# Optimization experiments

Hardware: AMD Instinct MI355X
Metric: run time of the kernel (lower is better)

The kernel has to match this reference:

```python
import jax, jax.numpy as jnp
import numpy as np

N = 50000      # nodes
E = 800000     # edges (avg degree 16)
F_IN = 256     # input feature dim
H, D = 4, 32   # heads, per-head dim
HD = H * D
K = 25000      # SAGPool keeps ceil(0.5*N) nodes
C = 2          # classes
SLOPE = 0.4
NEG = -1e9

def _gat(x, src, dst, valid, n, W, b, al, ar):
    # DGL GATConv: fc -> per-head attn logits -> edge softmax over dst -> weighted sum
    h = (x @ W).reshape(-1, H, D)                      # [n,H,D]
    el = jnp.einsum('nhd,hd->nh', h, al)
    er = jnp.einsum('nhd,hd->nh', h, ar)
    e = jax.nn.leaky_relu(el[src] + er[dst], SLOPE)    # [E,H]
    e = jnp.where(valid[:, None], e, NEG)
    m = jnp.maximum(jax.ops.segment_max(e, dst, num_segments=n), NEG)
    ex = jnp.exp(e - m[dst]) * valid[:, None].astype(x.dtype)
    s = jax.ops.segment_sum(ex, dst, num_segments=n)
    alpha = ex / jnp.maximum(s[dst], 1e-16)            # [E,H] edge softmax
    out = jax.ops.segment_sum(alpha[:, :, None] * h[src], dst, num_segments=n)
    return out + b.reshape(1, H, D), alpha

def _sagpool(x, src, dst, valid, n, k, Wc, bc):
    # score = GraphConv(in,1) with symmetric norm; keep top-k nodes, scale by tanh(score)
    vf = valid.astype(x.dtype)
    deg_o = jnp.maximum(jax.ops.segment_sum(vf, src, num_segments=n), 1.0)
    deg_i = jnp.maximum(jax.ops.segment_sum(vf, dst, num_segments=n), 1.0)
    h = (x @ Wc) * (deg_o ** -0.5)[:, None]
    agg = jax.ops.segment_sum(h[src] * vf[:, None], dst, num_segments=n)
    score = (agg * (deg_i ** -0.5)[:, None] + bc)[:, 0]   # [n]
    vals, perm = jax.lax.top_k(score, k)
    xk = x[perm] * jnp.tanh(vals)[:, None]                # [k,F]
    new_id = jnp.full((n,), -1, jnp.int32).at[perm].set(jnp.arange(k, dtype=jnp.int32))
    ns, nd = new_id[src], new_id[dst]
    nv = valid & (ns >= 0) & (nd >= 0)                    # edges fully inside subgraph
    return xk, jnp.where(nv, ns, 0), jnp.where(nv, nd, 0), nv

def setup_inputs():
    key = jax.random.key(0)
    k = jax.random.split(key, 18)
    rn = lambda i, shape, scale: jax.random.normal(k[i], shape, jnp.float32) * scale
    return {
        "feature": rn(0, (N, F_IN), 1.0),
        "strength": jax.random.uniform(k[1], (E,), dtype=jnp.float32),
        "W0": rn(2, (F_IN, HD), F_IN ** -0.5), "b0": jnp.zeros((HD,), jnp.float32),
        "al0": rn(3, (H, D), 0.1), "ar0": rn(4, (H, D), 0.1),
        "Wc0": rn(5, (HD, 1), HD ** -0.5), "bc0": jnp.zeros((1,), jnp.float32),
        "W1": rn(6, (HD, HD), HD ** -0.5), "b1": jnp.zeros((HD,), jnp.float32),
        "al1": rn(7, (H, D), 0.1), "ar1": rn(8, (H, D), 0.1),
        "gate_W": rn(9, (D, 1), D ** -0.5), "gate_b": jnp.zeros((1,), jnp.float32),
        "cls_W": rn(10, (D, C), D ** -0.5), "cls_b": jnp.zeros((C,), jnp.float32),
        "src": jax.random.randint(k[11], (E,), 0, N, dtype=jnp.int32),
        "dst": jax.random.randint(k[12], (E,), 0, N, dtype=jnp.int32),
    }

def reference(feature, strength, W0, b0, al0, ar0, Wc0, bc0, W1, b1, al1, ar1,
              gate_W, gate_b, cls_W, cls_b, src, dst):
    valid0 = jnp.ones((E,), bool)
    h0, _ = _gat(feature, src, dst, valid0, N, W0, b0, al0, ar0)
    x = h0.reshape(N, HD)                                  # flatten(1)
    x1, s1, d1, v1 = _sagpool(x, src, dst, valid0, N, K, Wc0, bc0)
    h1, atten = _gat(x1, s1, d1, v1, K, W1, b1, al1, ar1)  # get_attention=True
    strength1 = strength * v1.astype(strength.dtype)       # edata carried into subgraph (masked)
    res = h1.mean(axis=1)                                  # [K,D] mean over heads
    gate = jax.nn.softmax(res @ gate_W + gate_b, axis=0)   # [K,1] GlobalAttentionPooling
    readout = jnp.sum(gate * res, axis=0, keepdims=True)   # [1,D]
    lbl_pred = readout @ cls_W + cls_b                     # [1,C]
    return (readout, lbl_pred, atten, strength1)
```

## Files before the change

### kernel.cpp

```cpp
#include <hip/hip_runtime.h>
#include <stdint.h>

#define NN 50000
#define EE 800000
#define FIN 256
#define HD 128
#define DD 32
#define KK 25000
#define SLOPEF 0.4f
#define NEGF (-1e9f)
#define ATT_OFF 34
#define STR_OFF (34 + EE * 4)
#define CW 128

#define BCH 32
#define EPC (EE / BCH)

__device__ __forceinline__ unsigned fkey(float x) {
    unsigned u = __float_as_uint(x);
    return (u & 0x80000000u) ? ~u : (u | 0x80000000u);
}
__device__ __forceinline__ float unfkey(unsigned k) {
    unsigned u = (k & 0x80000000u) ? (k ^ 0x80000000u) : ~k;
    return __uint_as_float(u);
}
__device__ __forceinline__ float lrelu(float v) { return v > 0.f ? v : SLOPEF * v; }

struct P {
    const float *feature, *strength, *W0, *b0, *al0, *ar0, *Wc0, *bc0;
    const float *W1, *b1, *al1, *ar1, *gW, *gb, *cW, *cb;
    const int *src, *dst;
    double *Zacc, *racc;
    int *cnt;
    unsigned *gmaxk;
    unsigned *rs;
    unsigned *binsHi, *binsLo;
    unsigned *keys;
    unsigned char *degc_i, *degc_o;
    unsigned *cb0;
    int *dsum;
    int *csr_src, *rank, *off0, *sel, *slot, *list, *bsum, *boff;
    float *z0, *el0, *er0, *q4, *m0f, *s0f, *b0wc, *hc, *xk, *z1;
    float *el1, *er1, *m1f, *s1f, *res, *g, *tscale;
    float *out;
};

#define BM 128
#define BN 64
#define BK 16
__device__ void gemm_body(
    const float* __restrict__ A, const float* __restrict__ B, float* __restrict__ C,
    int M, int Kd,
    const float* __restrict__ al, const float* __restrict__ ar,
    float* __restrict__ el, float* __restrict__ er,
    const float* __restrict__ Wc, float* __restrict__ q4,
    int bx, int by) {
    __shared__ float As[BK][BM + 4];
    __shared__ float Bs[BK][BN];
    int bm = by * BM, bn = bx * BN;
    int tid = threadIdx.x;
    int tr = tid >> 4, tc = tid & 15;
    int lrow = tid >> 1;
    int arow = (bm + lrow < M) ? (bm + lrow) : -1;
    float acc[8][4] = {};
    for (int k0 = 0; k0 < Kd; k0 += BK) {
        {
            int col = (tid & 1) << 3;
            float4 v0 = {0.f,0.f,0.f,0.f}, v1 = {0.f,0.f,0.f,0.f};
            if (arow >= 0) {
                const float* ap = A + (size_t)arow * Kd + k0 + col;
                v0 = *(const float4*)ap; v1 = *(const float4*)(ap + 4);
            }
            As[col + 0][lrow] = v0.x; As[col + 1][lrow] = v0.y;
            As[col + 2][lrow] = v0.z; As[col + 3][lrow] = v0.w;
            As[col + 4][lrow] = v1.x; As[col + 5][lrow] = v1.y;
            As[col + 6][lrow] = v1.z; As[col + 7][lrow] = v1.w;
        }
        {
            int kr = tid >> 4, col = (tid & 15) << 2;
            float4 v = *(const float4*)(B + (size_t)(k0 + kr) * HD + bn + col);
            *(float4*)&Bs[kr][col] = v;
        }
        __syncthreads();
#pragma unroll
        for (int kk = 0; kk < BK; kk++) {
            float a[8], b[4];
#pragma unroll
            for (int i = 0; i < 8; i++) a[i] = As[kk][tr * 8 + i];
#pragma unroll
            for (int j = 0; j < 4; j++) b[j] = Bs[kk][tc * 4 + j];
#pragma unroll
            for (int i = 0; i < 8; i++)
#pragma unroll
                for (int j = 0; j < 4; j++) acc[i][j] = fmaf(a[i], b[j], acc[i][j]);
        }
        __syncthreads();
    }
#pragma unroll
    for (int i = 0; i < 8; i++) {
        int gr = bm + tr * 8 + i;
        if (gr < M) {
            float4 v = {acc[i][0], acc[i][1], acc[i][2], acc[i][3]};
            *(float4*)(C + (size_t)gr * HD + bn + tc * 4) = v;
        }
    }
    int head = bx * 2 + (tc >> 3);
    int dbase = (tc & 7) * 4;
    const float* alh = al + head * 32 + dbase;
    const float* arh = ar + head * 32 + dbase;
    float a0 = alh[0], a1 = alh[1], a2 = alh[2], a3 = alh[3];
    float r0 = arh[0], r1 = arh[1], r2 = arh[2], r3 = arh[3];
    float w0 = 0.f, w1 = 0.f, w2 = 0.f, w3 = 0.f;
    if (Wc) {
        const float* wch = Wc + head * 32 + dbase;
        w0 = wch[0]; w1 = wch[1]; w2 = wch[2]; w3 = wch[3];
    }
#pragma unroll
    for (int i = 0; i < 8; i++) {
        int gr = bm + tr * 8 + i;
        float pe = acc[i][0]*a0 + acc[i][1]*a1 + acc[i][2]*a2 + acc[i][3]*a3;
        float pr = acc[i][0]*r0 + acc[i][1]*r1 + acc[i][2]*r2 + acc[i][3]*r3;
        float pq = acc[i][0]*w0 + acc[i][1]*w1 + acc[i][2]*w2 + acc[i][3]*w3;
#pragma unroll
        for (int o = 1; o < 8; o <<= 1) {
            pe += __shfl_xor(pe, o); pr += __shfl_xor(pr, o); pq += __shfl_xor(pq, o);
        }
        if ((tc & 7) == 0 && gr < M) {
            el[gr * 4 + head] = pe; er[gr * 4 + head] = pr;
            if (Wc) q4[gr * 4 + head] = pq;
        }
    }
}

__global__ __launch_bounds__(256) void k_count0(P p) {
    __shared__ unsigned hist[NN / 4];
    int blk = blockIdx.x;
    int isD = blk < BCH;
    int c = isD ? blk : blk - BCH;
    for (int w = threadIdx.x; w < NN / 4; w += 256) hist[w] = 0u;
    __syncthreads();
    int j0 = c * EPC, j1 = j0 + EPC;
    if (isD) {
        for (int e = j0 + (int)threadIdx.x; e < j1; e += 256) {
            int d = p.dst[e];
            unsigned sh = (unsigned)(d & 3) * 8u;
            unsigned old = atomicAdd(&hist[d >> 2], 1u << sh);
            p.rank[e] = (int)((old >> sh) & 0xffu);
        }
    } else {
        for (int e = j0 + (int)threadIdx.x; e < j1; e += 256) {
            int s = p.src[e];
            atomicAdd(&hist[s >> 2], 1u << ((unsigned)(s & 3) * 8u));
        }
    }
    __syncthreads();
    unsigned* o32 = (unsigned*)((isD ? p.degc_i : p.degc_o) + (size_t)c * NN);
    for (int w = threadIdx.x; w < NN / 4; w += 256) o32[w] = hist[w];
}

__global__ __launch_bounds__(256) void k_bsum(const unsigned char* __restrict__ deg,
                                              int* __restrict__ bsum, int n, int nn) {
    int i = blockIdx.x * 256 + threadIdx.x;
    int v = 0;
    if (i < n) {
#pragma unroll
        for (int c = 0; c < BCH; c++) v += deg[(size_t)c * nn + i];
    }
    int lane = threadIdx.x & 63, w = threadIdx.x >> 6;
    __shared__ int ws[4];
#pragma unroll
    for (int o = 1; o < 64; o <<= 1) v += __shfl_xor(v, o);
    if (lane == 0) ws[w] = v;
    __syncthreads();
    if (threadIdx.x == 0) bsum[blockIdx.x] = ws[0] + ws[1] + ws[2] + ws[3];
}
__global__ __launch_bounds__(256) void k_bscan(const int* __restrict__ bsum, int nb,
                                               int* __restrict__ boff,
                                               int* __restrict__ off, int n) {
    __shared__ int ws[4];
    __shared__ int wo[5];
    int t = threadIdx.x;
    int v = (t < nb) ? bsum[t] : 0;
    int lane = t & 63, w = t >> 6;
    int incl = v;
    for (int o = 1; o < 64; o <<= 1) { int u = __shfl_up(incl, o); if (lane >= o) incl += u; }
    if (lane == 63) ws[w] = incl;
    __syncthreads();
    if (t == 0) { int a = 0; for (int i = 0; i < 4; i++) { wo[i] = a; a += ws[i]; } wo[4] = a; }
    __syncthreads();
    if (t < nb) boff[t] = wo[w] + incl - v;
    if (t == 0) off[n] = wo[4];
}
__global__ __launch_bounds__(256) void k_fscan0(P p) {
    __shared__ int ws[4];
    __shared__ int wo[4];
    int i = blockIdx.x * 256 + threadIdx.x;
    int v = 0;
    if (i < NN) {
#pragma unroll
        for (int c = 0; c < BCH; c++) v += p.degc_i[(size_t)c * NN + i];
    }
    int lane = threadIdx.x & 63, w = threadIdx.x >> 6;
    int incl = v;
    for (int o = 1; o < 64; o <<= 1) { int u = __shfl_up(incl, o); if (lane >= o) incl += u; }
    if (lane == 63) ws[w] = incl;
    __syncthreads();
    if (threadIdx.x == 0) { int a = 0; for (int k = 0; k < 4; k++) { wo[k] = a; a += ws[k]; } }
    __syncthreads();
    if (i < NN) {
        int base = p.boff[blockIdx.x] + wo[w] + incl - v;
        p.off0[i] = base;
        unsigned run = (unsigned)base;
        int s = 0;
#pragma unroll
        for (int c = 0; c < BCH; c++) {
            p.cb0[(size_t)c * NN + i] = run;
            run += p.degc_i[(size_t)c * NN + i];
            s += p.degc_o[(size_t)c * NN + i];
        }
        p.dsum[i] = s;
    }
}

#define G0B 782
#define GB_E 3125
__global__ __launch_bounds__(256) void k_g0sc(P p) {
    int blk = blockIdx.x;
    if (blk < G0B) {
        gemm_body(p.feature, p.W0, p.z0, NN, FIN, p.al0, p.ar0, p.el0, p.er0,
                  p.Wc0, p.q4, blk & 1, blk >> 1);
    } else if (blk < G0B + GB_E) {
        int e = (blk - G0B) * 256 + threadIdx.x;
        if (e < EE) {
            int c = e / EPC;
            int d = p.dst[e];
            unsigned pos = p.cb0[(size_t)c * NN + d] + (unsigned)p.rank[e];
            p.csr_src[pos] = p.src[e];
        }
    } else {
        int l = threadIdx.x;
        if (l < 64) {
            float t = p.b0[l] * p.Wc0[l] + p.b0[l + 64] * p.Wc0[l + 64];
#pragma unroll
            for (int o = 1; o < 64; o <<= 1) t += __shfl_xor(t, o);
            if (l == 0) p.b0wc[0] = t;
        }
    }
}

__global__ __launch_bounds__(256) void k_fgatlite(
    const int* __restrict__ off, const int* __restrict__ csrs,
    const float* __restrict__ el, const float* __restrict__ er,
    const float* __restrict__ q4, const int* __restrict__ dsum,
    const float* __restrict__ b0wc,
    float* __restrict__ hc, float* __restrict__ m0f, float* __restrict__ s0f) {
    int wv = threadIdx.x >> 6, lane = threadIdx.x & 63;
    int v = blockIdx.x * 4 + wv;
    int b = off[v], e = off[v + 1], deg = e - b;
    int h = lane >> 4, sub = lane & 15;
    float erh = er[(size_t)v * 4 + h];
    float m = NEGF;
    for (int li = sub; li < deg; li += 16) {
        int s = csrs[b + li];
        m = fmaxf(m, lrelu(el[(size_t)s * 4 + h] + erh));
    }
#pragma unroll
    for (int o = 1; o < 16; o <<= 1) m = fmaxf(m, __shfl_xor(m, o));
    float ssum = 0.f, hq = 0.f;
    for (int li = sub; li < deg; li += 16) {
        int s = csrs[b + li];
        float ex = expf(lrelu(el[(size_t)s * 4 + h] + erh) - m);
        ssum += ex;
        hq = fmaf(ex, q4[(size_t)s * 4 + h], hq);
    }
#pragma unroll
    for (int o = 1; o < 16; o <<= 1) { ssum += __shfl_xor(ssum, o); hq += __shfl_xor(hq, o); }
    if (sub == 0) { m0f[v * 4 + h] = m; s0f[v * 4 + h] = ssum; }
    float t = hq / fmaxf(ssum, 1e-16f);
    t += __shfl_xor(t, 16);
    t += __shfl_xor(t, 32);
    if (lane == 0)
        hc[v] = (t + b0wc[0]) / sqrtf(fmaxf((float)dsum[v], 1.f));
}

__global__ __launch_bounds__(256) void k_score(P p) {
    int v = blockIdx.x * blockDim.x + threadIdx.x;
    if (v >= NN) return;
    int b = p.off0[v], en = p.off0[v + 1];
    float acc = 0.f;
    for (int i = b; i < en; i++) acc += p.hc[p.csr_src[i]];
    float dg = fmaxf((float)(en - b), 1.f);
    float sc = acc / sqrtf(dg) + p.bc0[0];
    p.keys[v] = fkey(sc);
    p.sel[v] = 0;
}

#define HB 49
__global__ __launch_bounds__(1024) void k_h0(P p) {
    __shared__ unsigned hist[16384];
    int i = blockIdx.x * 1024 + (int)threadIdx.x;
    unsigned key = (i < NN) ? p.keys[i] : 0xFFFFFFFFu;
    unsigned b16 = key >> 16;
#pragma unroll
    for (int half = 0; half < 2; half++) {
        for (int w = threadIdx.x; w < 16384; w += 1024) hist[w] = 0u;
        __syncthreads();
        if (i < NN && (int)(b16 >> 15) == half) {
            unsigned bb = b16 & 0x7FFFu;
            atomicAdd(&hist[bb >> 1], 1u << (16u * (bb & 1u)));
        }
        __syncthreads();
        for (int w = threadIdx.x; w < 16384; w += 1024) {
            unsigned hv = hist[w];
            unsigned lo = hv & 0xFFFFu, hi = hv >> 16;
            if (lo) atomicAdd(&p.binsHi[half * 32768 + 2 * w], lo);
            if (hi) atomicAdd(&p.binsHi[half * 32768 + 2 * w + 1], hi);
        }
        __syncthreads();
    }
}

__global__ __launch_bounds__(1024) void k_h1(P p) {
    __shared__ unsigned hist[16384];
    int i = blockIdx.x * 1024 + (int)threadIdx.x;
    unsigned hib = p.rs[2];
    unsigned key = (i < NN) ? p.keys[i] : 0u;
    int cand = (i < NN) && ((key >> 16) == hib);
    unsigned b16 = key & 0xFFFFu;
#pragma unroll
    for (int half = 0; half < 2; half++) {
        for (int w = threadIdx.x; w < 16384; w += 1024) hist[w] = 0u;
        __syncthreads();
        if (cand && (int)(b16 >> 15) == half) {
            unsigned bb = b16 & 0x7FFFu;
            atomicAdd(&hist[bb >> 1], 1u << (16u * (bb & 1u)));
        }
        __syncthreads();
        for (int w = threadIdx.x; w < 16384; w += 1024) {
            unsigned hv = hist[w];
            unsigned lo = hv & 0xFFFFu, hi = hv >> 16;
            if (lo) atomicAdd(&p.binsLo[half * 32768 + 2 * w], lo);
            if (hi) atomicAdd(&p.binsLo[half * 32768 + 2 * w + 1], hi);
        }
        __syncthreads();
    }
}

__global__ __launch_bounds__(1024) void k_rsel2(P p, int level) {
    const unsigned* bins = level ? p.binsLo : p.binsHi;
    int K = level ? (int)p.rs[3] : KK;
    __shared__ unsigned wsm[16];
    __shared__ unsigned wpre[17];
    int t = threadIdx.x;
    unsigned base = (unsigned)t * 64;
    const uint4* b4 = (const uint4*)(bins + base);
    unsigned S = 0;
#pragma unroll
    for (int i = 0; i < 16; i++) {
        uint4 u = b4[i];
        S += u.x + u.y + u.z + u.w;
    }
    int lane = t & 63, w = t >> 6;
    unsigned val = S;
    for (int o = 1; o < 64; o <<= 1) { unsigned u = __shfl_up(val, o); if (lane >= o) val += u; }
    if (lane == 63) wsm[w] = val;
    __syncthreads();
    if (t == 0) { unsigned a = 0; for (int i = 0; i < 16; i++) { wpre[i] = a; a += wsm[i]; } wpre[16] = a; }
    __syncthreads();
    unsigned incl = wpre[w] + val;
    unsigned running = wpre[16] - incl;
    for (int i = 63; i >= 0; i--) {
        unsigned c = bins[base + i];
        unsigned above = running;
        running += c;
        if ((int)above < K && (int)running >= K) {
            if (level == 0) { p.rs[2] = base + (unsigned)i; p.rs[3] = (unsigned)(K - (int)above); }
            else { p.rs[0] = (p.rs[2] << 16) | (base + (unsigned)i); p.rs[1] = (unsigned)(K - (int)above); }
        }
    }
}

__global__ __launch_bounds__(1024) void k_ties(P p) {
    __shared__ int base;
    __shared__ int wsums[16];
    unsigned pivot = p.rs[0];
    int need = (int)p.rs[1];
    if (threadIdx.x == 0) base = 0;
    __syncthreads();
    for (int st = 0; st < NN; st += 1024) {
        int v = st + (int)threadIdx.x;
        int flag = (v < NN && p.keys[v] == pivot) ? 1 : 0;
        unsigned long long m = __ballot(flag);
        int lane = threadIdx.x & 63, w = threadIdx.x >> 6;
        int pre = __popcll(m & ((1ull << lane) - 1ull));
        if (lane == 0) wsums[w] = __popcll(m);
        __syncthreads();
        int woff = 0;
        for (int i = 0; i < w; i++) woff += wsums[i];
        int rank = base + woff + pre;
        if (flag && rank < need) p.sel[v] = 1;
        __syncthreads();
        if (threadIdx.x == 0) {
            int s = 0;
            for (int i = 0; i < 16; i++) s += wsums[i];
            base += s;
        }
        __syncthreads();
    }
}

__global__ void k_list(P p) {
    int v = blockIdx.x * blockDim.x + threadIdx.x;
    if (v >= NN) return;
    unsigned k = p.keys[v];
    int selv = (k > p.rs[0]) || p.sel[v];
    if (selv) {
        int i = atomicAdd(p.cnt, 1);
        p.list[i] = v;
        p.slot[v] = i;
        p.tscale[i] = tanhf(unfkey(k));
    } else {
        p.slot[v] = -1;
    }
}

__global__ __launch_bounds__(256) void k_fgatx(
    const int* __restrict__ list, const float* __restrict__ tscale,
    const int* __restrict__ off, const int* __restrict__ csrs,
    const float* __restrict__ el, const float* __restrict__ er,
    const float* __restrict__ m0f, const float* __restrict__ s0f,
    const float* __restrict__ z, const float* __restrict__ b0,
    float* __restrict__ xk) {
    __shared__ int ssrc[4][CW];
    __shared__ float sexp[4][CW][4];
    int wv = threadIdx.x >> 6, lane = threadIdx.x & 63;
    int i = blockIdx.x * 4 + wv;
    int v = list[i];
    int b = off[v], e = off[v + 1], deg = e - b;
    int h = lane >> 4, sub = lane & 15;
    float erh = er[(size_t)v * 4 + h];
    float mh = m0f[v * 4 + h];
    for (int li = sub; li < deg; li += 16) {
        int s = csrs[b + li];
        if (h == 0 && li < CW) ssrc[wv][li] = s;
        if (li < CW) sexp[wv][li][h] = expf(lrelu(el[(size_t)s * 4 + h] + erh) - mh);
    }
    __syncthreads();
    int h0 = lane >> 5, h1 = h0 + 2;
    float s0 = s0f[v * 4 + h0], s1 = s0f[v * 4 + h1];
    float m0 = m0f[v * 4 + h0], m1 = m0f[v * 4 + h1];
    float er0v = er[(size_t)v * 4 + h0], er1v = er[(size_t)v * 4 + h1];
    int c0 = lane, c1 = lane + 64;
    float acc0 = 0.f, acc1 = 0.f;
    for (int li = 0; li < deg; li++) {
        int s; float w0, w1;
        if (li < CW) {
            s = ssrc[wv][li];
            w0 = sexp[wv][li][h0]; w1 = sexp[wv][li][h1];
        } else {
            s = csrs[b + li];
            w0 = expf(lrelu(el[(size_t)s * 4 + h0] + er0v) - m0);
            w1 = expf(lrelu(el[(size_t)s * 4 + h1] + er1v) - m1);
        }
        int su = __builtin_amdgcn_readfirstlane(s);
        const float* zr = z + (size_t)su * HD;
        acc0 = fmaf(w0, zr[c0], acc0);
        acc1 = fmaf(w1, zr[c1], acc1);
    }
    float ts = tscale[i];
    float* xr = xk + (size_t)i * HD;
    xr[c0] = (acc0 / fmaxf(s0, 1e-16f) + b0[c0]) * ts;
    xr[c1] = (acc1 / fmaxf(s1, 1e-16f) + b0[c1]) * ts;
}

#define G1B 392
__global__ __launch_bounds__(256) void k_gemm1(P p) {
    gemm_body(p.xk, p.W1, p.z1, KK, HD, p.al1, p.ar1, p.el1, p.er1,
              nullptr, nullptr, blockIdx.x & 1, blockIdx.x >> 1);
}

__global__ __launch_bounds__(256) void k_fgat2(P p) {
    __shared__ int ssrc[4][CW];
    __shared__ float sexp[4][CW][4];
    int wv = threadIdx.x >> 6, lane = threadIdx.x & 63;
    int i = blockIdx.x * 4 + wv;
    int v = p.list[i];
    int b = p.off0[v], e = p.off0[v + 1], deg = e - b;
    int h = lane >> 4, sub = lane & 15;
    float4 er4 = *(const float4*)(p.er1 + (size_t)i * 4);
    float erh = ((const float*)&er4)[h];
    float m = NEGF;
    for (int li = sub; li < deg; li += 16) {
        int so = p.csr_src[b + li];
        int ss = p.slot[so];
        if (h == 0 && li < CW) ssrc[wv][li] = ss;
        if (ss >= 0) m = fmaxf(m, lrelu(p.el1[(size_t)ss * 4 + h] + erh));
    }
#pragma unroll
    for (int o = 1; o < 16; o <<= 1) m = fmaxf(m, __shfl_xor(m, o));
    float ssum = 0.f;
    for (int li = sub; li < deg; li += 16) {
        int so = p.csr_src[b + li];
        int ss = p.slot[so];
        float x = (ss >= 0) ? expf(lrelu(p.el1[(size_t)ss * 4 + h] + erh) - m) : 0.f;
        if (li < CW) sexp[wv][li][h] = x;
        ssum += x;
    }
#pragma unroll
    for (int o = 1; o < 16; o <<= 1) ssum += __shfl_xor(ssum, o);
    if (sub == 0) { p.m1f[i * 4 + h] = m; p.s1f[i * 4 + h] = ssum; }
    __syncthreads();
    int h0 = lane >> 5, h1 = h0 + 2;
    float m0 = __shfl(m, h0 << 4), m1 = __shfl(m, h1 << 4);
    float s0 = __shfl(ssum, h0 << 4), s1 = __shfl(ssum, h1 << 4);
    int c0 = lane, c1 = lane + 64;
    float acc0 = 0.f, acc1 = 0.f;
    for (int li = 0; li < deg; li++) {
        int s; float w0, w1;
        if (li < CW) {
            s = ssrc[wv][li];
            if (s < 0) continue;
            w0 = sexp[wv][li][h0]; w1 = sexp[wv][li][h1];
        } else {
            int so = p.csr_src[b + li];
            s = p.slot[so];
            if (s < 0) continue;
            w0 = expf(lrelu(p.el1[(size_t)s * 4 + h0] + ((const float*)&er4)[h0]) - m0);
            w1 = expf(lrelu(p.el1[(size_t)s * 4 + h1] + ((const float*)&er4)[h1]) - m1);
        }
        int su = __builtin_amdgcn_readfirstlane(s);
        const float* zr = p.z1 + (size_t)su * HD;
        acc0 = fmaf(w0, zr[c0], acc0);
        acc1 = fmaf(w1, zr[c1], acc1);
    }
    float xc0 = acc0 / fmaxf(s0, 1e-16f) + p.b1[c0];
    float xc1 = acc1 / fmaxf(s1, 1e-16f) + p.b1[c1];
    float t = xc0 + xc1;
    t += __shfl_xor(t, 32);
    float pg = 0.f;
    if (lane < 32) {
        float r = 0.25f * t;
        p.res[(size_t)i * 32 + lane] = r;
        pg = r * p.gW[lane];
    }
#pragma unroll
    for (int o = 1; o < 32; o <<= 1) pg += __shfl_xor(pg, o);
    if (lane == 0) p.g[i] = pg + p.gb[0];
}

__global__ void k_ealpha1(P p) {
    int e = blockIdx.x * blockDim.x + threadIdx.x;
    if (e >= EE) return;
    int ds = p.slot[p.src[e]], dd = p.slot[p.dst[e]];
    float a[4] = {0.f, 0.f, 0.f, 0.f};
    float st = 0.f;
    if (ds >= 0 && dd >= 0) {
        float4 es = *(const float4*)(p.el1 + ds * 4);
        float4 ed = *(const float4*)(p.er1 + dd * 4);
        float l[4] = {lrelu(es.x + ed.x), lrelu(es.y + ed.y), lrelu(es.z + ed.z), lrelu(es.w + ed.w)};
#pragma unroll
        for (int h = 0; h < 4; h++) {
            float m = p.m1f[dd * 4 + h];
            float ex = expf(l[h] - m);
            a[h] = ex / fmaxf(p.s1f[dd * 4 + h], 1e-16f);
        }
        st = p.strength[e];
    }
    float* o = p.out + ATT_OFF + (size_t)e * 4;
    *(float2*)(o) = make_float2(a[0], a[1]);
    *(float2*)(o + 2) = make_float2(a[2], a[3]);
    p.out[STR_OFF + e] = st;
}

__global__ void k_gmax(P p) {
    __shared__ float red[256];
    int t = threadIdx.x;
    float m = -3.4e38f;
    for (int i = blockIdx.x * 256 + t; i < KK; i += gridDim.x * 256) m = fmaxf(m, p.g[i]);
    red[t] = m;
    __syncthreads();
    for (int o = 128; o > 0; o >>= 1) { if (t < o) red[t] = fmaxf(red[t], red[t + o]); __syncthreads(); }
    if (t == 0) atomicMax(p.gmaxk, fkey(red[0]));
}
#define WSUM_BLOCKS 104
__global__ __launch_bounds__(256) void k_wsum(P p) {
    __shared__ double vred[256];
    __shared__ double zred[8];
    int t = threadIdx.x, il = t >> 5, d = t & 31;
    float gm = unfkey(*p.gmaxk);
    double accv = 0.0, accw = 0.0;
    for (int i = blockIdx.x * 8 + il; i < KK; i += WSUM_BLOCKS * 8) {
        float w = expf(p.g[i] - gm);
        accv += (double)(w * p.res[(size_t)i * 32 + d]);
        if (d == 0) accw += (double)w;
    }
    vred[t] = accv;
    if (d == 0) zred[il] = accw;
    __syncthreads();
    if (il == 0) {
        double s = 0;
#pragma unroll
        for (int k2 = 0; k2 < 8; k2++) s += vred[k2 * 32 + d];
        atomicAdd(&p.racc[d], s);
    }
    if (t == 32) {
        double z2 = 0;
#pragma unroll
        for (int k2 = 0; k2 < 8; k2++) z2 += zred[k2];
        atomicAdd(p.Zacc, z2);
    }
}
__global__ void k_final(P p) {
    __shared__ float rb[32];
    int t = threadIdx.x;
    double Z = *p.Zacc;
    if (t < 32) {
        float r = (float)(p.racc[t] / Z);
        p.out[t] = r;
        rb[t] = r;
    }
    __syncthreads();
    if (t < 2) {
        float s = 0.f;
        for (int d = 0; d < 32; d++) s += rb[d] * p.cW[d * 2 + t];
        p.out[32 + t] = s + p.cb[t];
    }
}

extern "C" void kernel_launch(void* const* d_in, const int* in_sizes, int n_in,
                              void* d_out, int out_size, void* d_ws, size_t ws_size,
                              hipStream_t stream) {
    (void)in_sizes; (void)n_in; (void)out_size; (void)ws_size;
    P p;
    p.feature  = (const float*)d_in[0];
    p.strength = (const float*)d_in[1];
    p.W0  = (const float*)d_in[2];  p.b0  = (const float*)d_in[3];
    p.al0 = (const float*)d_in[4];  p.ar0 = (const float*)d_in[5];
    p.Wc0 = (const float*)d_in[6];  p.bc0 = (const float*)d_in[7];
    p.W1  = (const float*)d_in[8];  p.b1  = (const float*)d_in[9];
    p.al1 = (const float*)d_in[10]; p.ar1 = (const float*)d_in[11];
    p.gW  = (const float*)d_in[12]; p.gb  = (const float*)d_in[13];
    p.cW  = (const float*)d_in[14]; p.cb  = (const float*)d_in[15];
    p.src = (const int*)d_in[16];   p.dst = (const int*)d_in[17];
    p.out = (float*)d_out;

    char* ws = (char*)d_ws;
    size_t off = 0;
    auto alloc = [&](size_t bytes) -> void* {
        void* r = ws + off;
        off = (off + bytes + 255) & ~(size_t)255;
        return r;
    };
    p.Zacc  = (double*)alloc(8);
    p.racc  = (double*)alloc(32 * 8);
    p.cnt   = (int*)alloc(4);
    p.gmaxk = (unsigned*)alloc(4);
    p.rs    = (unsigned*)alloc(16);
    p.binsHi = (unsigned*)alloc(65536 * 4);
    p.binsLo = (unsigned*)alloc(65536 * 4);
    size_t zbytes = off;
    p.degc_i = (unsigned char*)alloc((size_t)BCH * NN);
    p.degc_o = (unsigned char*)alloc((size_t)BCH * NN);
    p.cb0 = (unsigned*)alloc((size_t)BCH * NN * 4);
    p.dsum = (int*)alloc((size_t)NN * 4);
    p.z0 = (float*)alloc((size_t)NN * HD * 4);
    p.xk = (float*)alloc((size_t)KK * HD * 4);
    p.z1 = (float*)alloc((size_t)KK * HD * 4);
    p.csr_src = (int*)alloc((size_t)EE * 4);
    p.rank    = (int*)alloc((size_t)EE * 4);
    p.el0 = (float*)alloc((size_t)NN * 4 * 4);
    p.er0 = (float*)alloc((size_t)NN * 4 * 4);
    p.q4  = (float*)alloc((size_t)NN * 4 * 4);
    p.m0f = (float*)alloc((size_t)NN * 4 * 4);
    p.s0f = (float*)alloc((size_t)NN * 4 * 4);
    p.b0wc = (float*)alloc(4);
    p.off0 = (int*)alloc((size_t)(NN + 1) * 4);
    p.bsum = (int*)alloc(256 * 4);
    p.boff = (int*)alloc(256 * 4);
    p.hc    = (float*)alloc((size_t)NN * 4);
    p.keys  = (unsigned*)alloc((size_t)NN * 4);
    p.sel   = (int*)alloc((size_t)NN * 4);
    p.slot  = (int*)alloc((size_t)NN * 4);
    p.list  = (int*)alloc((size_t)KK * 4);
    p.tscale = (float*)alloc((size_t)KK * 4);
    p.el1 = (float*)alloc((size_t)KK * 4 * 4);
    p.er1 = (float*)alloc((size_t)KK * 4 * 4);
    p.m1f = (float*)alloc((size_t)KK * 4 * 4);
    p.s1f = (float*)alloc((size_t)KK * 4 * 4);
    p.res = (float*)alloc((size_t)KK * DD * 4);
    p.g   = (float*)alloc((size_t)KK * 4);

    const int GB_N = (NN + 255) / 256;

    hipMemsetAsync(d_ws, 0, zbytes, stream);

    k_count0<<<2 * BCH, 256, 0, stream>>>(p);
    k_bsum<<<GB_N, 256, 0, stream>>>(p.degc_i, p.bsum, NN, NN);
    k_bscan<<<1, 256, 0, stream>>>(p.bsum, GB_N, p.boff, p.off0, NN);
    k_fscan0<<<GB_N, 256, 0, stream>>>(p);
    k_g0sc<<<G0B + GB_E + 1, 256, 0, stream>>>(p);
    k_fgatlite<<<NN / 4, 256, 0, stream>>>(p.off0, p.csr_src, p.el0, p.er0, p.q4,
                                           p.dsum, p.b0wc, p.hc, p.m0f, p.s0f);

    k_score<<<GB_N, 256, 0, stream>>>(p);
    k_h0<<<HB, 1024, 0, stream>>>(p);
    k_rsel2<<<1, 1024, 0, stream>>>(p, 0);
    k_h1<<<HB, 1024, 0, stream>>>(p);
    k_rsel2<<<1, 1024, 0, stream>>>(p, 1);
    k_ties<<<1, 1024, 0, stream>>>(p);
    k_list<<<GB_N, 256, 0, stream>>>(p);

    k_fgatx<<<KK / 4, 256, 0, stream>>>(p.list, p.tscale, p.off0, p.csr_src,
                                        p.el0, p.er0, p.m0f, p.s0f, p.z0, p.b0, p.xk);
    k_gemm1<<<G1B, 256, 0, stream>>>(p);
    k_fgat2<<<KK / 4, 256, 0, stream>>>(p);
    k_ealpha1<<<GB_E, 256, 0, stream>>>(p);

    k_gmax<<<98, 256, 0, stream>>>(p);
    k_wsum<<<WSUM_BLOCKS, 256, 0, stream>>>(p);
    k_final<<<1, 64, 0, stream>>>(p);
}
```

Baseline: 579.7 us.

## Parallelize degree counting, tie selection, and fuse edge-alpha with gate max

After: 532.6 us. 8.1% less time.

```diff
diff --git a/kernel.cpp b/kernel.cpp
--- a/kernel.cpp
+++ b/kernel.cpp
@@ -15,6 +15,7 @@
 
 #define BCH 32
 #define EPC (EE / BCH)
+#define NRQ 12500
 
 __device__ __forceinline__ unsigned fkey(float x) {
     unsigned u = __float_as_uint(x);
@@ -39,7 +40,7 @@
     unsigned char *degc_i, *degc_o;
     unsigned *cb0;
     int *dsum;
-    int *csr_src, *rank, *off0, *sel, *slot, *list, *bsum, *boff;
+    int *csr_src, *rank, *off0, *slot, *list, *bsum, *boff;
     float *z0, *el0, *er0, *q4, *m0f, *s0f, *b0wc, *hc, *xk, *z1;
     float *el1, *er1, *m1f, *s1f, *res, *g, *tscale;
     float *out;
@@ -133,29 +134,33 @@
 }
 
 __global__ __launch_bounds__(256) void k_count0(P p) {
-    __shared__ unsigned hist[NN / 4];
+    __shared__ unsigned hist[NRQ / 4];
     int blk = blockIdx.x;
-    int isD = blk < BCH;
-    int c = isD ? blk : blk - BCH;
-    for (int w = threadIdx.x; w < NN / 4; w += 256) hist[w] = 0u;
+    int isD = blk < 128;
+    int c = blk & 31, rq = (blk >> 5) & 3;
+    int nbase = rq * NRQ;
+    for (int w = threadIdx.x; w < NRQ / 4; w += 256) hist[w] = 0u;
     __syncthreads();
     int j0 = c * EPC, j1 = j0 + EPC;
     if (isD) {
         for (int e = j0 + (int)threadIdx.x; e < j1; e += 256) {
-            int d = p.dst[e];
-            unsigned sh = (unsigned)(d & 3) * 8u;
-            unsigned old = atomicAdd(&hist[d >> 2], 1u << sh);
-            p.rank[e] = (int)((old >> sh) & 0xffu);
+            int d = p.dst[e] - nbase;
+            if ((unsigned)d < (unsigned)NRQ) {
+                unsigned sh = (unsigned)(d & 3) * 8u;
+                unsigned old = atomicAdd(&hist[d >> 2], 1u << sh);
+                p.rank[e] = (int)((old >> sh) & 0xffu);
+            }
         }
     } else {
         for (int e = j0 + (int)threadIdx.x; e < j1; e += 256) {
-            int s = p.src[e];
-            atomicAdd(&hist[s >> 2], 1u << ((unsigned)(s & 3) * 8u));
-        }
-    }
-    __syncthreads();
-    unsigned* o32 = (unsigned*)((isD ? p.degc_i : p.degc_o) + (size_t)c * NN);
-    for (int w = threadIdx.x; w < NN / 4; w += 256) o32[w] = hist[w];
+            int s = p.src[e] - nbase;
+            if ((unsigned)s < (unsigned)NRQ)
+                atomicAdd(&hist[s >> 2], 1u << ((unsigned)(s & 3) * 8u));
+        }
+    }
+    __syncthreads();
+    unsigned* o32 = (unsigned*)((isD ? p.degc_i : p.degc_o) + (size_t)c * NN + nbase);
+    for (int w = threadIdx.x; w < NRQ / 4; w += 256) o32[w] = hist[w];
 }
 
 __global__ __launch_bounds__(256) void k_bsum(const unsigned char* __restrict__ deg,
@@ -222,21 +227,22 @@
     }
 }
 
+#define GB_E 3125
+__global__ __launch_bounds__(256) void k_scat0(P p) {
+    int e = blockIdx.x * 256 + threadIdx.x;
+    if (e >= EE) return;
+    int c = e / EPC;
+    int d = p.dst[e];
+    unsigned pos = p.cb0[(size_t)c * NN + d] + (unsigned)p.rank[e];
+    p.csr_src[pos] = p.src[e];
+}
+
 #define G0B 782
-#define GB_E 3125
-__global__ __launch_bounds__(256) void k_g0sc(P p) {
+__global__ __launch_bounds__(256) void k_gemm0(P p) {
     int blk = blockIdx.x;
     if (blk < G0B) {
         gemm_body(p.feature, p.W0, p.z0, NN, FIN, p.al0, p.ar0, p.el0, p.er0,
                   p.Wc0, p.q4, blk & 1, blk >> 1);
-    } else if (blk < G0B + GB_E) {
-        int e = (blk - G0B) * 256 + threadIdx.x;
-        if (e < EE) {
-            int c = e / EPC;
-            int d = p.dst[e];
-            unsigned pos = p.cb0[(size_t)c * NN + d] + (unsigned)p.rank[e];
-            p.csr_src[pos] = p.src[e];
-        }
     } else {
         int l = threadIdx.x;
         if (l < 64) {
@@ -292,7 +298,6 @@
     float dg = fmaxf((float)(en - b), 1.f);
     float sc = acc / sqrtf(dg) + p.bc0[0];
     p.keys[v] = fkey(sc);
-    p.sel[v] = 0;
 }
 
 #define HB 49
@@ -380,47 +385,48 @@
     }
 }
 
-__global__ __launch_bounds__(1024) void k_ties(P p) {
-    __shared__ int base;
-    __shared__ int wsums[16];
+__global__ __launch_bounds__(256) void k_tcnt(P p) {
+    __shared__ int ws[4];
+    int v = blockIdx.x * 256 + (int)threadIdx.x;
+    int flag = (v < NN && p.keys[v] == p.rs[0]) ? 1 : 0;
+    unsigned long long m = __ballot(flag);
+    int lane = threadIdx.x & 63, w = threadIdx.x >> 6;
+    if (lane == 0) ws[w] = __popcll(m);
+    __syncthreads();
+    if (threadIdx.x == 0) p.bsum[blockIdx.x] = ws[0] + ws[1] + ws[2] + ws[3];
+}
+
+__global__ __launch_bounds__(256) void k_list(P p) {
+    __shared__ int pre0;
+    __shared__ int ws[4];
+    int blk = blockIdx.x, tid = threadIdx.x;
     unsigned pivot = p.rs[0];
     int need = (int)p.rs[1];
-    if (threadIdx.x == 0) base = 0;
-    __syncthreads();
-    for (int st = 0; st < NN; st += 1024) {
-        int v = st + (int)threadIdx.x;
-        int flag = (v < NN && p.keys[v] == pivot) ? 1 : 0;
-        unsigned long long m = __ballot(flag);
-        int lane = threadIdx.x & 63, w = threadIdx.x >> 6;
-        int pre = __popcll(m & ((1ull << lane) - 1ull));
-        if (lane == 0) wsums[w] = __popcll(m);
-        __syncthreads();
-        int woff = 0;
-        for (int i = 0; i < w; i++) woff += wsums[i];
-        int rank = base + woff + pre;
-        if (flag && rank < need) p.sel[v] = 1;
-        __syncthreads();
-        if (threadIdx.x == 0) {
-            int s = 0;
-            for (int i = 0; i < 16; i++) s += wsums[i];
-            base += s;
-        }
-        __syncthreads();
-    }
-}
-
-__global__ void k_list(P p) {
-    int v = blockIdx.x * blockDim.x + threadIdx.x;
-    if (v >= NN) return;
-    unsigned k = p.keys[v];
-    int selv = (k > p.rs[0]) || p.sel[v];
-    if (selv) {
-        int i = atomicAdd(p.cnt, 1);
-        p.list[i] = v;
-        p.slot[v] = i;
-        p.tscale[i] = tanhf(unfkey(k));
-    } else {
-        p.slot[v] = -1;
+    int v = blk * 256 + tid;
+    unsigned k = (v < NN) ? p.keys[v] : 0u;
+    int flag = (v < NN && k == pivot) ? 1 : 0;
+    unsigned long long mask = __ballot(flag);
+    int lane = tid & 63, w = tid >> 6;
+    if (lane == 0) ws[w] = __popcll(mask);
+    if (tid == 0) {
+        int s = 0;
+        for (int b2 = 0; b2 < blk; b2++) s += p.bsum[b2];
+        pre0 = s;
+    }
+    __syncthreads();
+    int woff = 0;
+    for (int i = 0; i < w; i++) woff += ws[i];
+    int rank = pre0 + woff + __popcll(mask & ((1ull << lane) - 1ull));
+    if (v < NN) {
+        int selv = (k > pivot) || (flag && rank < need);
+        if (selv) {
+            int idx = atomicAdd(p.cnt, 1);
+            p.list[idx] = v;
+            p.slot[v] = idx;
+            p.tscale[idx] = tanhf(unfkey(k));
+        } else {
+            p.slot[v] = -1;
+        }
     }
 }
 
@@ -548,40 +554,42 @@
     if (lane == 0) p.g[i] = pg + p.gb[0];
 }
 
-__global__ void k_ealpha1(P p) {
-    int e = blockIdx.x * blockDim.x + threadIdx.x;
-    if (e >= EE) return;
-    int ds = p.slot[p.src[e]], dd = p.slot[p.dst[e]];
-    float a[4] = {0.f, 0.f, 0.f, 0.f};
-    float st = 0.f;
-    if (ds >= 0 && dd >= 0) {
-        float4 es = *(const float4*)(p.el1 + ds * 4);
-        float4 ed = *(const float4*)(p.er1 + dd * 4);
-        float l[4] = {lrelu(es.x + ed.x), lrelu(es.y + ed.y), lrelu(es.z + ed.z), lrelu(es.w + ed.w)};
-#pragma unroll
-        for (int h = 0; h < 4; h++) {
-            float m = p.m1f[dd * 4 + h];
-            float ex = expf(l[h] - m);
-            a[h] = ex / fmaxf(p.s1f[dd * 4 + h], 1e-16f);
-        }
-        st = p.strength[e];
-    }
-    float* o = p.out + ATT_OFF + (size_t)e * 4;
-    *(float2*)(o) = make_float2(a[0], a[1]);
-    *(float2*)(o + 2) = make_float2(a[2], a[3]);
-    p.out[STR_OFF + e] = st;
-}
-
-__global__ void k_gmax(P p) {
-    __shared__ float red[256];
-    int t = threadIdx.x;
-    float m = -3.4e38f;
-    for (int i = blockIdx.x * 256 + t; i < KK; i += gridDim.x * 256) m = fmaxf(m, p.g[i]);
-    red[t] = m;
-    __syncthreads();
-    for (int o = 128; o > 0; o >>= 1) { if (t < o) red[t] = fmaxf(red[t], red[t + o]); __syncthreads(); }
-    if (t == 0) atomicMax(p.gmaxk, fkey(red[0]));
-}
+__global__ __launch_bounds__(256) void k_eg(P p) {
+    int blk = blockIdx.x;
+    if (blk < GB_E) {
+        int e = blk * 256 + (int)threadIdx.x;
+        if (e >= EE) return;
+        int ds = p.slot[p.src[e]], dd = p.slot[p.dst[e]];
+        float a[4] = {0.f, 0.f, 0.f, 0.f};
+        float st = 0.f;
+        if (ds >= 0 && dd >= 0) {
+            float4 es = *(const float4*)(p.el1 + ds * 4);
+            float4 ed = *(const float4*)(p.er1 + dd * 4);
+            float l[4] = {lrelu(es.x + ed.x), lrelu(es.y + ed.y), lrelu(es.z + ed.z), lrelu(es.w + ed.w)};
+#pragma unroll
+            for (int h = 0; h < 4; h++) {
+                float m = p.m1f[dd * 4 + h];
+                float ex = expf(l[h] - m);
+                a[h] = ex / fmaxf(p.s1f[dd * 4 + h], 1e-16f);
+            }
+            st = p.strength[e];
+        }
+        float* o = p.out + ATT_OFF + (size_t)e * 4;
+        *(float2*)(o) = make_float2(a[0], a[1]);
+        *(float2*)(o + 2) = make_float2(a[2], a[3]);
+        p.out[STR_OFF + e] = st;
+    } else {
+        __shared__ float red[256];
+        int t = threadIdx.x;
+        float m = -3.4e38f;
+        for (int i = (blk - GB_E) * 256 + t; i < KK; i += 98 * 256) m = fmaxf(m, p.g[i]);
+        red[t] = m;
+        __syncthreads();
+        for (int o = 128; o > 0; o >>= 1) { if (t < o) red[t] = fmaxf(red[t], red[t + o]); __syncthreads(); }
+        if (t == 0) atomicMax(p.gmaxk, fkey(red[0]));
+    }
+}
+
 #define WSUM_BLOCKS 104
 __global__ __launch_bounds__(256) void k_wsum(P p) {
     __shared__ double vred[256];
@@ -679,7 +687,6 @@
     p.boff = (int*)alloc(256 * 4);
     p.hc    = (float*)alloc((size_t)NN * 4);
     p.keys  = (unsigned*)alloc((size_t)NN * 4);
-    p.sel   = (int*)alloc((size_t)NN * 4);
     p.slot  = (int*)alloc((size_t)NN * 4);
     p.list  = (int*)alloc((size_t)KK * 4);
     p.tscale = (float*)alloc((size_t)KK * 4);
@@ -694,11 +701,12 @@
 
     hipMemsetAsync(d_ws, 0, zbytes, stream);
 
-    k_count0<<<2 * BCH, 256, 0, stream>>>(p);
+    k_count0<<<256, 256, 0, stream>>>(p);
     k_bsum<<<GB_N, 256, 0, stream>>>(p.degc_i, p.bsum, NN, NN);
     k_bscan<<<1, 256, 0, stream>>>(p.bsum, GB_N, p.boff, p.off0, NN);
     k_fscan0<<<GB_N, 256, 0, stream>>>(p);
-    k_g0sc<<<G0B + GB_E + 1, 256, 0, stream>>>(p);
+    k_scat0<<<GB_E, 256, 0, stream>>>(p);
+    k_gemm0<<<G0B + 1, 256, 0, stream>>>(p);
     k_fgatlite<<<NN / 4, 256, 0, stream>>>(p.off0, p.csr_src, p.el0, p.er0, p.q4,
                                            p.dsum, p.b0wc, p.hc, p.m0f, p.s0f);
 
@@ -707,16 +715,15 @@
     k_rsel2<<<1, 1024, 0, stream>>>(p, 0);
     k_h1<<<HB, 1024, 0, stream>>>(p);
     k_rsel2<<<1, 1024, 0, stream>>>(p, 1);
-    k_ties<<<1, 1024, 0, stream>>>(p);
+    k_tcnt<<<GB_N, 256, 0, stream>>>(p);
     k_list<<<GB_N, 256, 0, stream>>>(p);
 
     k_fgatx<<<KK / 4, 256, 0, stream>>>(p.list, p.tscale, p.off0, p.csr_src,
                                         p.el0, p.er0, p.m0f, p.s0f, p.z0, p.b0, p.xk);
     k_gemm1<<<G1B, 256, 0, stream>>>(p);
     k_fgat2<<<KK / 4, 256, 0, stream>>>(p);
-    k_ealpha1<<<GB_E, 256, 0, stream>>>(p);
-
-    k_gmax<<<98, 256, 0, stream>>>(p);
+
+    k_eg<<<GB_E + 98, 256, 0, stream>>>(p);
     k_wsum<<<WSUM_BLOCKS, 256, 0, stream>>>(p);
     k_final<<<1, 64, 0, stream>>>(p);
 }
```
